# Kernel tuning notes

Hardware: AMD Instinct MI355X
Metric: run time of the kernel (lower is better)

The kernel has to match this reference:

```python
import jax, jax.numpy as jnp
import numpy as np

B, T, W, D = 2, 64, 32, 512
H = 8                      # n_heads
N = 64                     # d_state
EXPAND = 2
DIN = EXPAND * D           # 1024 d_inner
R = -(-D // 16)            # dt_rank = ceil(d_model/16) = 32
K = 4                      # d_conv (mamba default)


def setup_inputs():
    key = jax.random.key(0)
    ks = jax.random.split(key, 20)
    s = 0.02
    inp = {
        'x': jax.random.normal(ks[0], (B, T, W, D), jnp.float32),
        'wq': jax.random.normal(ks[1], (D, D), jnp.float32) * s,
        'bq': jnp.zeros((D,), jnp.float32),
        'wk': jax.random.normal(ks[2], (D, D), jnp.float32) * s,
        'bk': jnp.zeros((D,), jnp.float32),
        'wv': jax.random.normal(ks[3], (D, D), jnp.float32) * s,
        'bv': jnp.zeros((D,), jnp.float32),
        'wo': jax.random.normal(ks[4], (D, D), jnp.float32) * s,
        'bo': jnp.zeros((D,), jnp.float32),
        'in_proj_w': jax.random.normal(ks[5], (2 * DIN, D), jnp.float32) * s,
        'conv_w': jax.random.normal(ks[6], (DIN, 1, K), jnp.float32) * 0.2,
        'conv_b': jnp.zeros((DIN,), jnp.float32),
        'x_proj_w': jax.random.normal(ks[7], (R + 2 * N, DIN), jnp.float32) * s,
        'dt_proj_w': jax.random.normal(ks[8], (DIN, R), jnp.float32) * 0.1,
        'dt_proj_b': jnp.full((DIN,), -4.6, jnp.float32),  # ~softplus^-1(0.01)
        'A_log': jnp.log(jnp.broadcast_to(jnp.arange(1, N + 1, dtype=jnp.float32), (DIN, N))),
        'D_param': jnp.ones((DIN,), jnp.float32),
        'out_proj_w': jax.random.normal(ks[9], (D, DIN), jnp.float32) * s,
        'ln_w': jnp.ones((D,), jnp.float32),
        'ln_b': jnp.zeros((D,), jnp.float32),
    }
    return inp


def _attention(xf, wq, bq, wk, bk, wv, bv, wo, bo):
    b, L, d = xf.shape
    e = d // H
    q = (xf @ wq.T + bq).reshape(b, L, H, e)
    k = (xf @ wk.T + bk).reshape(b, L, H, e)
    v = (xf @ wv.T + bv).reshape(b, L, H, e)
    scale = 1.0 / jnp.sqrt(jnp.float32(e))
    scores = jnp.einsum('blhe,bshe->bhls', q, k) * scale
    causal = jnp.tril(jnp.ones((L, L), bool))
    scores = jnp.where(causal, scores, jnp.finfo(scores.dtype).min)
    attn = jax.nn.softmax(scores, axis=-1)  # dropout off (eval mode)
    out = jnp.einsum('bhls,bshe->blhe', attn, v).reshape(b, L, d)
    return out @ wo.T + bo


def _mamba(xf, in_proj_w, conv_w, conv_b, x_proj_w, dt_proj_w, dt_proj_b,
           A_log, D_param, out_proj_w):
    b, L, d = xf.shape
    xz = xf @ in_proj_w.T                 # (B,L,2*DIN)
    x_in, z = jnp.split(xz, 2, axis=-1)
    # causal depthwise conv1d over L
    xc = jnp.transpose(x_in, (0, 2, 1))   # (B,DIN,L)
    xc = jax.lax.conv_general_dilated(
        xc, conv_w, window_strides=(1,), padding=[(K - 1, 0)],
        feature_group_count=DIN, dimension_numbers=('NCH', 'OIH', 'NCH'))
    xc = xc + conv_b[None, :, None]
    u = jax.nn.silu(jnp.transpose(xc, (0, 2, 1)))   # (B,L,DIN)
    dbc = u @ x_proj_w.T                             # (B,L,R+2N)
    dt, Bm, Cm = dbc[..., :R], dbc[..., R:R + N], dbc[..., R + N:]
    dt = jax.nn.softplus(dt @ dt_proj_w.T + dt_proj_b)  # (B,L,DIN)
    A = -jnp.exp(A_log)                                 # (DIN,N)

    def step(h, t):
        dt_t, B_t, C_t, u_t = t  # (b,DIN),(b,N),(b,N),(b,DIN)
        dA = jnp.exp(dt_t[..., None] * A)                       # (b,DIN,N)
        h = dA * h + (dt_t * u_t)[..., None] * B_t[:, None, :]  # (b,DIN,N)
        y = jnp.einsum('bdn,bn->bd', h, C_t)
        return h, y

    h0 = jnp.zeros((b, DIN, N), xf.dtype)
    xs = (jnp.swapaxes(dt, 0, 1), jnp.swapaxes(Bm, 0, 1),
          jnp.swapaxes(Cm, 0, 1), jnp.swapaxes(u, 0, 1))
    _, ys = jax.lax.scan(step, h0, xs)
    y = jnp.swapaxes(ys, 0, 1) + u * D_param   # (B,L,DIN)
    y = y * jax.nn.silu(z)
    return y @ out_proj_w.T


def reference(x, wq, bq, wk, bk, wv, bv, wo, bo, in_proj_w, conv_w, conv_b,
              x_proj_w, dt_proj_w, dt_proj_b, A_log, D_param, out_proj_w,
              ln_w, ln_b):
    b, t, w, d = x.shape
    L = t * w
    xf = x.reshape(b, L, d)
    x_attn = _attention(xf, wq, bq, wk, bk, wv, bv, wo, bo).reshape(b, t, w, d)
    x_mamba = _mamba(xf, in_proj_w, conv_w, conv_b, x_proj_w, dt_proj_w,
                     dt_proj_b, A_log, D_param, out_proj_w).reshape(b, t, w, d)
    h = x + x_attn + x_mamba
    mu = jnp.mean(h, axis=-1, keepdims=True)
    var = jnp.mean(jnp.square(h - mu), axis=-1, keepdims=True)
    return (h - mu) * jax.lax.rsqrt(var + 1e-5) * ln_w + ln_b
```

## Files before the change

kernel.cpp:

```cpp
#include <hip/hip_runtime.h>

typedef __attribute__((ext_vector_type(4))) float f32x4;
typedef __attribute__((ext_vector_type(8))) short short8;
typedef __attribute__((ext_vector_type(2))) unsigned uint2e;

#define DEV static __device__ __forceinline__

DEV ushort f2b(float f) {
  union { float f; unsigned u; } v; v.f = f;
  unsigned r = v.u + 0x7FFF + ((v.u >> 16) & 1);
  return (ushort)(r >> 16);
}
DEV unsigned pack_bf2(float lo, float hi) {
  return (unsigned)f2b(lo) | ((unsigned)f2b(hi) << 16);
}
DEV float bflo(unsigned p) { return __uint_as_float(p << 16); }
DEV float bfhi(unsigned p) { return __uint_as_float(p & 0xFFFF0000u); }

DEV float fexp2(float x) { float r; asm("v_exp_f32 %0, %1" : "=v"(r) : "v"(x)); return r; }

DEV float xor32_add_lo(float s) {
  uint2e r = __builtin_amdgcn_permlane32_swap(__float_as_uint(s), __float_as_uint(s), false, false);
  return s + __uint_as_float(r.x);
}

#define QP(x, ctrl) __int_as_float(__builtin_amdgcn_update_dpp(0, __float_as_int(x), (ctrl), 0xf, 0xf, false))
#define SWZ(x, off) __int_as_float(__builtin_amdgcn_ds_swizzle(__float_as_int(x), (off)))
#define DPP_ADD(x, ctrl, rmask) \
  ((x) + __int_as_float(__builtin_amdgcn_update_dpp(0, __float_as_int(x), (ctrl), (rmask), 0xf, false)))

#define BB    2
#define LL    2048
#define DD    512
#define HH    8
#define EE    64
#define DIN   1024
#define NS    64
#define RR    32
#define BL    4096
#define NCH   16
#define TC    128
#define NC    1536
#define MFMA(a,b,c) __builtin_amdgcn_mfma_f32_16x16x32_bf16((a),(b),(c),0,0,0)

struct CvtJobs {
  const float* src[7];
  ushort*      dst[7];
  int          n[7];
};

__global__ __launch_bounds__(256) void cvt_multi(CvtJobs j) {
  int job = blockIdx.y;
  const float* s = j.src[job];
  ushort* d = j.dst[job];
  int n = j.n[job];
  for (int i = blockIdx.x * 256 + threadIdx.x; i < n; i += gridDim.x * 256)
    d[i] = f2b(s[i]);
}

__global__ __launch_bounds__(256) void pack_wcomb(
    const float* __restrict__ wo, const float* __restrict__ opw,
    const float* __restrict__ bq, const float* __restrict__ bk,
    const float* __restrict__ bv, ushort* __restrict__ wc,
    float* __restrict__ bqkv)
{
  int i = blockIdx.x * 256 + threadIdx.x;
  if (i < NC) bqkv[i] = (i < DD) ? bq[i] : ((i < 2 * DD) ? bk[i - DD] : bv[i - 2 * DD]);
  if (i >= DD * NC) return;
  int n = i / NC, c = i - n * NC;
  float v = (c < DD) ? wo[n * DD + c] : opw[n * DIN + (c - DD)];
  wc[i] = f2b(v);
}

__global__ __launch_bounds__(256) void gemm_bt(
    const ushort* __restrict__ A, const ushort* __restrict__ W,
    const float* __restrict__ bias, float* __restrict__ outF,
    ushort* __restrict__ outB, int M, int N, int K, int act)
{
  __shared__ ushort As[64][40];
  __shared__ ushort Ws[64][40];
  int m0 = blockIdx.y * 64, n0 = blockIdx.x * 64;
  int tid = threadIdx.x, l = tid & 63, w = tid >> 6;
  int wm = (w >> 1) * 32, wn = (w & 1) * 32;
  int lr = l & 15, kl = (l >> 4) * 8;
  int srow = tid >> 2, sk = (tid & 3) * 8;
  f32x4 acc[2][2] = {};

  for (int k0 = 0; k0 < K; k0 += 32) {
    uint4 av = *(const uint4*)&A[(size_t)(m0 + srow) * K + k0 + sk];
    uint4 wv;
    if (n0 + srow < N) wv = *(const uint4*)&W[(size_t)(n0 + srow) * K + k0 + sk];
    else { wv.x = 0; wv.y = 0; wv.z = 0; wv.w = 0; }
    *(uint4*)&As[srow][sk] = av;
    *(uint4*)&Ws[srow][sk] = wv;
    __syncthreads();
    short8 a0 = *(const short8*)&As[wm + lr][kl];
    short8 a1 = *(const short8*)&As[wm + 16 + lr][kl];
    short8 b0 = *(const short8*)&Ws[wn + lr][kl];
    short8 b1 = *(const short8*)&Ws[wn + 16 + lr][kl];
    acc[0][0] = MFMA(a0, b0, acc[0][0]);
    acc[0][1] = MFMA(a0, b1, acc[0][1]);
    acc[1][0] = MFMA(a1, b0, acc[1][0]);
    acc[1][1] = MFMA(a1, b1, acc[1][1]);
    __syncthreads();
  }

  #pragma unroll
  for (int mi = 0; mi < 2; mi++)
    #pragma unroll
    for (int ni = 0; ni < 2; ni++) {
      int rbase = m0 + wm + mi * 16 + ((l >> 4) << 2);
      int col = n0 + wn + ni * 16 + lr;
      if (col < N) {
        float bval = bias ? bias[col] : 0.f;
        #pragma unroll
        for (int r = 0; r < 4; r++) {
          float v = acc[mi][ni][r] + bval;
          if (act == 1) v = (v > 20.f) ? v : log1pf(__expf(v));
          size_t o = (size_t)(rbase + r) * N + col;
          if (outF) outF[o] = v;
          if (outB) outB[o] = f2b(v);
        }
      }
    }
}

__global__ __launch_bounds__(256) void gemm128(
    const ushort* __restrict__ A, const ushort* __restrict__ W,
    const float* __restrict__ bias, float* __restrict__ outF,
    ushort* __restrict__ outB, int M, int N, int K)
{
  __shared__ ushort As[128][40];
  __shared__ ushort Ws[128][40];
  int tid = threadIdx.x, l = tid & 63, w = tid >> 6;
  int m0 = blockIdx.y * 128, n0 = blockIdx.x * 128;
  int wm = (w >> 1) * 64, wn = (w & 1) * 64;
  int lr = l & 15, kl = (l >> 4) * 8;
  int srow = tid >> 1, sk = (tid & 1) * 16;
  f32x4 acc[4][4] = {};

  const ushort* Ap = A + (size_t)(m0 + srow) * K + sk;
  const ushort* Wp = W + (size_t)(n0 + srow) * K + sk;

  for (int k0 = 0; k0 < K; k0 += 32) {
    uint4 a0 = *(const uint4*)(Ap);
    uint4 a1 = *(const uint4*)(Ap + 8);
    uint4 b0 = *(const uint4*)(Wp);
    uint4 b1 = *(const uint4*)(Wp + 8);
    __syncthreads();
    *(uint4*)&As[srow][sk]     = a0;
    *(uint4*)&As[srow][sk + 8] = a1;
    *(uint4*)&Ws[srow][sk]     = b0;
    *(uint4*)&Ws[srow][sk + 8] = b1;
    __syncthreads();
    short8 af[4], bf[4];
    #pragma unroll
    for (int mi = 0; mi < 4; mi++) af[mi] = *(const short8*)&As[wm + mi * 16 + lr][kl];
    #pragma unroll
    for (int ni = 0; ni < 4; ni++) bf[ni] = *(const short8*)&Ws[wn + ni * 16 + lr][kl];
    #pragma unroll
    for (int mi = 0; mi < 4; mi++)
      #pragma unroll
      for (int ni = 0; ni < 4; ni++)
        acc[mi][ni] = MFMA(af[mi], bf[ni], acc[mi][ni]);
    Ap += 32; Wp += 32;
  }

  #pragma unroll
  for (int mi = 0; mi < 4; mi++)
    #pragma unroll
    for (int ni = 0; ni < 4; ni++) {
      int rbase = m0 + wm + mi * 16 + ((l >> 4) << 2);
      int col = n0 + wn + ni * 16 + lr;
      float bval = bias ? bias[col] : 0.f;
      #pragma unroll
      for (int r = 0; r < 4; r++) {
        float v = acc[mi][ni][r] + bval;
        size_t o = (size_t)(rbase + r) * N + col;
        if (outF) outF[o] = v;
        if (outB) outB[o] = f2b(v);
      }
    }
}

__global__ __launch_bounds__(256) void flash_attn(
    const ushort* __restrict__ qkv, ushort* __restrict__ comb)
{
  __shared__ ushort Qs[64][72];
  __shared__ ushort Ks[64][72];
  __shared__ ushort Vt[64][72];
  __shared__ ushort Ps[64][72];

  int qt = 31 - blockIdx.x;
  int h = blockIdx.y, b = blockIdx.z;
  int tid = threadIdx.x, l = tid & 63, w = tid >> 6;
  int w16 = w * 16, lr = l & 15, kl = (l >> 4) * 8;

  for (int i = tid; i < 512; i += 256) {
    int row = i >> 3, c8 = (i & 7) * 8;
    *(uint4*)&Qs[row][c8] =
        *(const uint4*)&qkv[((size_t)(b * LL + qt * 64 + row)) * NC + h * EE + c8];
  }
  __syncthreads();

  float m_r[4] = {-1e30f, -1e30f, -1e30f, -1e30f};
  float l_r[4] = {0.f, 0.f, 0.f, 0.f};
  f32x4 oacc[4] = {};

  for (int kv = 0; kv <= qt; kv++) {
    for (int i = tid; i < 512; i += 256) {
      int s = i >> 3, c8 = (i & 7) * 8;
      size_t rb = ((size_t)(b * LL + kv * 64 + s)) * NC + h * EE + c8;
      *(uint4*)&Ks[s][c8] = *(const uint4*)&qkv[rb + DD];
      uint4 vv = *(const uint4*)&qkv[rb + 2 * DD];
      const ushort* pv = (const ushort*)&vv;
      #pragma unroll
      for (int jj = 0; jj < 8; jj++) Vt[c8 + jj][s] = pv[jj];
    }
    __syncthreads();

    f32x4 sacc[4] = {};
    #pragma unroll
    for (int kk = 0; kk < 2; kk++) {
      short8 aq = *(const short8*)&Qs[w16 + lr][kk * 32 + kl];
      #pragma unroll
      for (int nt = 0; nt < 4; nt++) {
        short8 bk8 = *(const short8*)&Ks[nt * 16 + lr][kk * 32 + kl];
        sacc[nt] = MFMA(aq, bk8, sacc[nt]);
      }
    }

    bool diag = (kv == qt);
    float scl[4];
    #pragma unroll
    for (int r = 0; r < 4; r++) {
      int rloc = w16 + ((l >> 4) << 2) + r;
      float sv[4];
      #pragma unroll
      for (int nt = 0; nt < 4; nt++) {
        float v = sacc[nt][r] * 0.125f;
        if (diag && (nt * 16 + lr) > rloc) v = -1e30f;
        sv[nt] = v;
      }
      float mx = fmaxf(fmaxf(sv[0], sv[1]), fmaxf(sv[2], sv[3]));
      #pragma unroll
      for (int o = 1; o < 16; o <<= 1) mx = fmaxf(mx, __shfl_xor(mx, o));
      float mnew = fmaxf(m_r[r], mx);
      float sc = __expf(m_r[r] - mnew);
      float rs = 0.f;
      #pragma unroll
      for (int nt = 0; nt < 4; nt++) {
        float p = __expf(sv[nt] - mnew);
        rs += p;
        Ps[rloc][nt * 16 + lr] = f2b(p);
      }
      #pragma unroll
      for (int o = 1; o < 16; o <<= 1) rs += __shfl_xor(rs, o);
      l_r[r] = l_r[r] * sc + rs;
      m_r[r] = mnew;
      scl[r] = sc;
    }
    #pragma unroll
    for (int nt = 0; nt < 4; nt++)
      #pragma unroll
      for (int r = 0; r < 4; r++) oacc[nt][r] *= scl[r];

    #pragma unroll
    for (int kk = 0; kk < 2; kk++) {
      short8 ap = *(const short8*)&Ps[w16 + lr][kk * 32 + kl];
      #pragma unroll
      for (int nt = 0; nt < 4; nt++) {
        short8 bv8 = *(const short8*)&Vt[nt * 16 + lr][kk * 32 + kl];
        oacc[nt] = MFMA(ap, bv8, oacc[nt]);
      }
    }
    __syncthreads();
  }

  #pragma unroll
  for (int nt = 0; nt < 4; nt++)
    #pragma unroll
    for (int r = 0; r < 4; r++) {
      int row = qt * 64 + w16 + ((l >> 4) << 2) + r;
      float v = oacc[nt][r] / l_r[r];
      comb[((size_t)(b * LL + row)) * NC + h * EE + nt * 16 + lr] = f2b(v);
    }
}

__global__ __launch_bounds__(256) void conv_silu(
    const float* __restrict__ xz, const float* __restrict__ cw,
    const float* __restrict__ cb, float* __restrict__ u, ushort* __restrict__ ub)
{
  int i = blockIdx.x * 256 + threadIdx.x;
  if (i >= BL * DIN) return;
  int d = i & (DIN - 1);
  int bl = i >> 10;
  int t = bl & (LL - 1);
  int b = bl >> 11;
  float s = cb[d];
  #pragma unroll
  for (int j = 0; j < 4; j++) {
    int tt = t - 3 + j;
    if (tt >= 0) s += xz[((size_t)(b * LL + tt)) * (2 * DIN) + d] * cw[d * 4 + j];
  }
  float r = s / (1.f + __expf(-s));
  u[i] = r;
  ub[i] = f2b(r);
}

__global__ __launch_bounds__(256) void slice_dt(
    const float* __restrict__ dbc, ushort* __restrict__ dtc)
{
  int i = blockIdx.x * 256 + threadIdx.x;
  if (i >= BL * RR) return;
  int m = i >> 5, r = i & 31;
  dtc[i] = f2b(dbc[m * 160 + r]);
}

__global__ __launch_bounds__(256) void pack_bc(
    const float* __restrict__ dbc, unsigned* __restrict__ bbp,
    float4* __restrict__ bcp4)
{
  int i = blockIdx.x * 256 + threadIdx.x;
  if (i >= BB * (LL / 2) * NS) return;
  int n = i & 63, tp = (i >> 6) & 1023, b = i >> 16;
  size_t r0 = ((size_t)(b * LL + 2 * tp)) * 160;
  float B0 = dbc[r0 + 32 + n],  C0 = dbc[r0 + 96 + n];
  float B1 = dbc[r0 + 192 + n], C1 = dbc[r0 + 256 + n];
  bbp[i] = pack_bf2(B0, B1);
  bcp4[i] = make_float4(B0, C0, B1, C1);
}

__global__ __launch_bounds__(256) void pack_dtu(
    const float* __restrict__ dtf, const float* __restrict__ uf,
    const float* __restrict__ xz, const float* __restrict__ dpar,
    unsigned* __restrict__ dtu_p, unsigned* __restrict__ sg_p)
{
  __shared__ float s_dt[32][65], s_du[32][65], s_gz[32][65], s_ug[32][65];
  int d0 = blockIdx.x * 64, t0 = blockIdx.y * 32;
  int tid = threadIdx.x;
  int c = tid & 63, r4 = tid >> 6;
  float Dv = dpar[d0 + c];
  #pragma unroll
  for (int k = 0; k < 8; k++) {
    int r = k * 4 + r4;
    size_t row = (size_t)(t0 + r);
    float dtv = dtf[row * DIN + d0 + c];
    float uv  = uf [row * DIN + d0 + c];
    float zz  = xz [row * (2 * DIN) + DIN + d0 + c];
    float g = zz / (1.f + __expf(-zz));
    s_dt[r][c] = dtv;
    s_du[r][c] = dtv * uv;
    s_gz[r][c] = g;
    s_ug[r][c] = uv * Dv * g;
  }
  __syncthreads();
  int dl = tid >> 2, q = tid & 3;
  int b = t0 >> 11, tl0 = t0 & (LL - 1);
  size_t obase = ((size_t)(b * DIN + d0 + dl)) * LL + tl0 + q * 8;
  #pragma unroll
  for (int tt = 0; tt < 8; tt++) {
    int t = q * 8 + tt;
    dtu_p[obase + tt] = pack_bf2(s_dt[t][dl], s_du[t][dl]);
    sg_p [obase + tt] = pack_bf2(s_gz[t][dl], s_ug[t][dl]);
  }
}

__global__ __launch_bounds__(256) void scan_phase1(
    const unsigned* __restrict__ dtu_p, const unsigned* __restrict__ bbp,
    const float* __restrict__ alog, float* __restrict__ hf, float* __restrict__ ap)
{
  __shared__ float lds[4][TC][2];
  int tid = threadIdx.x, w = tid >> 6, l = tid & 63;
  int wid = blockIdx.x * 4 + w;
  int d = wid & (DIN - 1);
  int c = (wid >> 10) & (NCH - 1);
  int b = wid >> 14;
  float An2 = -__expf(alog[d * NS + l]) * 1.44269504f;

  size_t pbase = ((size_t)(b * DIN + d)) * LL + c * TC;
  unsigned p0 = dtu_p[pbase + l];
  unsigned p1 = dtu_p[pbase + 64 + l];
  float s0 = bflo(p0), s1 = bflo(p1);
  s0 = DPP_ADD(s0, 0x111, 0xf); s0 = DPP_ADD(s0, 0x112, 0xf);
  s0 = DPP_ADD(s0, 0x114, 0xf); s0 = DPP_ADD(s0, 0x118, 0xf);
  s0 = DPP_ADD(s0, 0x142, 0xa); s0 = DPP_ADD(s0, 0x143, 0xc);
  s1 = DPP_ADD(s1, 0x111, 0xf); s1 = DPP_ADD(s1, 0x112, 0xf);
  s1 = DPP_ADD(s1, 0x114, 0xf); s1 = DPP_ADD(s1, 0x118, 0xf);
  s1 = DPP_ADD(s1, 0x142, 0xa); s1 = DPP_ADD(s1, 0x143, 0xc);
  float T0 = __uint_as_float(__builtin_amdgcn_readlane(__float_as_uint(s0), 63));
  float T  = T0 + __uint_as_float(__builtin_amdgcn_readlane(__float_as_uint(s1), 63));
  lds[w][l][0]      = T - s0;
  lds[w][l][1]      = bfhi(p0);
  lds[w][64 + l][0] = (T - T0) - s1;
  lds[w][64 + l][1] = bfhi(p1);
  __syncthreads();

  const unsigned* bq = bbp + ((size_t)(b * 1024 + c * 64) * 64 + l);
  float h0 = 0.f, h1 = 0.f;
  for (int g = 0; g < 16; g++) {
    unsigned bv[4];
    #pragma unroll
    for (int k = 0; k < 4; k++) bv[k] = bq[k * 64];
    const float* gb = &lds[w][g * 8][0];
    #pragma unroll
    for (int j = 0; j < 8; j++) {
      float2 dd = *(const float2*)(gb + j * 2);
      float Bv = (j & 1) ? bfhi(bv[j >> 1]) : bflo(bv[j >> 1]);
      float a = fexp2(dd.x * An2);
      if (j & 1) h1 += a * (dd.y * Bv);
      else       h0 += a * (dd.y * Bv);
    }
    bq += 256;
  }
  size_t o = (((size_t)((b << 10) + d) * NCH) + c) * 64 + l;
  hf[o] = h0 + h1;
  ap[o] = fexp2(T * An2);
}

__global__ __launch_bounds__(256) void scan_carry(
    const float* __restrict__ hf, const float* __restrict__ ap,
    float* __restrict__ carry)
{
  int i = blockIdx.x * 256 + threadIdx.x;
  int n = i & 63;
  int d = (i >> 6) & (DIN - 1);
  int b = i >> 16;
  size_t base = ((size_t)((b << 10) + d) * NCH) * 64 + n;
  float cur = 0.f;
  #pragma unroll
  for (int c = 0; c < NCH; c++) {
    carry[base + (size_t)c * 64] = cur;
    cur = ap[base + (size_t)c * 64] * cur + hf[base + (size_t)c * 64];
  }
}

__global__ __launch_bounds__(256) void scan_phase3(
    const unsigned* __restrict__ dtu_p, const unsigned* __restrict__ sg_p,
    const float4* __restrict__ bcp4, const float* __restrict__ alog,
    const float* __restrict__ carry, ushort* __restrict__ ymt)
{
  __shared__ float lds[4][TC][4];
  __shared__ ushort yt[4][TC];
  int tid = threadIdx.x, w = tid >> 6, l = tid & 63;
  int wid = blockIdx.x * 4 + w;
  int d = wid & (DIN - 1);
  int c = (wid >> 10) & (NCH - 1);
  int b = wid >> 14;
  float An2 = -__expf(alog[d * NS + l]) * 1.44269504f;

  size_t pbase = ((size_t)(b * DIN + d)) * LL + c * TC;
  #pragma unroll
  for (int q = 0; q < 2; q++) {
    unsigned pd = dtu_p[pbase + q * 64 + l];
    unsigned pg = sg_p [pbase + q * 64 + l];
    lds[w][q * 64 + l][0] = bflo(pd);
    lds[w][q * 64 + l][1] = bfhi(pd);
    lds[w][q * 64 + l][2] = bflo(pg);
    lds[w][q * 64 + l][3] = bfhi(pg);
  }
  __syncthreads();

  float h = carry[(((size_t)((b << 10) + d) * NCH) + c) * 64 + l];
  const float4* bq = bcp4 + ((size_t)(b * 1024 + c * 64) * 64 + l);
  bool s1f = l & 1, s2f = l & 2, s4f = l & 4;
  bool wl = l < 8;

  for (int g = 0; g < 16; g++) {
    float4 bcs[4];
    bcs[0] = bq[0]; bcs[1] = bq[64]; bcs[2] = bq[128]; bcs[3] = bq[192];
    const float* gb = &lds[w][g * 8][0];
    float p[8];
    #pragma unroll
    for (int j = 0; j < 8; j++) {
      float2 dd = *(const float2*)(gb + j * 4);
      float Bv = (j & 1) ? bcs[j >> 1].z : bcs[j >> 1].x;
      float Cv = (j & 1) ? bcs[j >> 1].w : bcs[j >> 1].y;
      float a = fexp2(dd.x * An2);
      h = a * h + dd.y * Bv;
      p[j] = h * Cv;
    }
    #pragma unroll
    for (int j = 0; j < 8; j++) p[j] += QP(p[j], 0xB1);
    float q0 = s1f ? p[1] : p[0];
    float q1 = s1f ? p[3] : p[2];
    float q2 = s1f ? p[5] : p[4];
    float q3 = s1f ? p[7] : p[6];
    q0 += QP(q0, 0x4E); q1 += QP(q1, 0x4E);
    q2 += QP(q2, 0x4E); q3 += QP(q3, 0x4E);
    float r0 = s2f ? q1 : q0;
    float r1 = s2f ? q3 : q2;
    r0 += SWZ(r0, 0x101F); r1 += SWZ(r1, 0x101F);
    float s = s4f ? r1 : r0;
    s += QP(s, 0x128);
    s += SWZ(s, 0x401F);
    s = xor32_add_lo(s);

    float2 sgv = *(const float2*)(&lds[w][g * 8 + (l & 7)][2]);
    if (wl) yt[w][g * 8 + l] = f2b(s * sgv.x + sgv.y);
    bq += 256;
  }
  __syncthreads();
  unsigned vv = *(const unsigned*)&yt[w][2 * l];
  ((unsigned*)(ymt + pbase))[l] = vv;
}

__global__ __launch_bounds__(256) void transpose_ym(
    const ushort* __restrict__ ymt, ushort* __restrict__ comb)
{
  __shared__ ushort tile[64][72];
  int tid = threadIdx.x;
  int bx = blockIdx.x;
  int by = blockIdx.y;
  int b  = blockIdx.z;
  int r = tid >> 2, c16 = (tid & 3) * 16;
  const ushort* src = ymt + ((size_t)(b * DIN + bx * 64 + r)) * LL + by * 64 + c16;
  *(uint4*)&tile[r][c16]     = *(const uint4*)src;
  *(uint4*)&tile[r][c16 + 8] = *(const uint4*)(src + 8);
  __syncthreads();
  ushort tmp[16];
  #pragma unroll
  for (int j = 0; j < 16; j++) tmp[j] = tile[c16 + j][r];
  ushort* dst = comb + ((size_t)(b * LL + by * 64 + r)) * NC + DD + bx * 64 + c16;
  *(uint4*)dst       = *(uint4*)&tmp[0];
  *(uint4*)(dst + 8) = *(uint4*)&tmp[8];
}

__global__ __launch_bounds__(256) void residual_ln(
    const float* __restrict__ x, const float* __restrict__ so,
    const float* __restrict__ lw, const float* __restrict__ lb,
    float* __restrict__ out)
{
  int row = blockIdx.x * 4 + (threadIdx.x >> 6);
  int l = threadIdx.x & 63;
  size_t base = (size_t)row * DD;
  float h[8];
  float s = 0.f, s2 = 0.f;
  #pragma unroll
  for (int half = 0; half < 2; half++) {
    int c = half * 256 + l * 4;
    float4 xv = *(const float4*)(x + base + c);
    float4 sv = *(const float4*)(so + base + c);
    float* hp = h + half * 4;
    hp[0] = xv.x + sv.x;
    hp[1] = xv.y + sv.y;
    hp[2] = xv.z + sv.z;
    hp[3] = xv.w + sv.w;
    #pragma unroll
    for (int j = 0; j < 4; j++) { s += hp[j]; s2 += hp[j] * hp[j]; }
  }
  #pragma unroll
  for (int o = 1; o < 64; o <<= 1) { s += __shfl_xor(s, o); s2 += __shfl_xor(s2, o); }
  float mean = s * (1.f / DD);
  float var = s2 * (1.f / DD) - mean * mean;
  float rs = rsqrtf(var + 1e-5f);
  #pragma unroll
  for (int half = 0; half < 2; half++) {
    int c = half * 256 + l * 4;
    float4 ov;
    ov.x = (h[half*4+0] - mean) * rs * lw[c+0] + lb[c+0];
    ov.y = (h[half*4+1] - mean) * rs * lw[c+1] + lb[c+1];
    ov.z = (h[half*4+2] - mean) * rs * lw[c+2] + lb[c+2];
    ov.w = (h[half*4+3] - mean) * rs * lw[c+3] + lb[c+3];
    *(float4*)(out + base + c) = ov;
  }
}

extern "C" void kernel_launch(void* const* d_in, const int* in_sizes, int n_in,
                              void* d_out, int out_size, void* d_ws, size_t ws_size,
                              hipStream_t stream) {
  const float* x    = (const float*)d_in[0];
  const float* wq   = (const float*)d_in[1];
  const float* bq   = (const float*)d_in[2];
  const float* wk   = (const float*)d_in[3];
  const float* bk   = (const float*)d_in[4];
  const float* wv   = (const float*)d_in[5];
  const float* bv   = (const float*)d_in[6];
  const float* wo   = (const float*)d_in[7];
  const float* bo   = (const float*)d_in[8];
  const float* inw  = (const float*)d_in[9];
  const float* cw   = (const float*)d_in[10];
  const float* cb   = (const float*)d_in[11];
  const float* xpw  = (const float*)d_in[12];
  const float* dtw  = (const float*)d_in[13];
  const float* dtb  = (const float*)d_in[14];
  const float* alog = (const float*)d_in[15];
  const float* dpar = (const float*)d_in[16];
  const float* opw  = (const float*)d_in[17];
  const float* lnw  = (const float*)d_in[18];
  const float* lnb  = (const float*)d_in[19];

  char* ws = (char*)d_ws;
  size_t off = 0;
  auto alloc = [&](size_t bytes) -> void* {
    void* p = ws + off;
    off += (bytes + 255) & ~(size_t)255;
    return p;
  };

  const size_t BLD = (size_t)BL * DD;
  const size_t BLDIN = (size_t)BL * DIN;
  const size_t BLNC = (size_t)BL * NC;

  ushort* xf_b   = (ushort*)alloc(BLD * 2);
  ushort* wqkv_b = (ushort*)alloc((size_t)NC * DD * 2);
  float*  bqkv   = (float*)alloc(NC * 4);
  ushort* inw_b  = (ushort*)alloc(2 * DIN * DD * 2);
  ushort* xpw_b  = (ushort*)alloc(160 * DIN * 2);
  ushort* dtw_b  = (ushort*)alloc(DIN * RR * 2);
  ushort* wcomb_b= (ushort*)alloc((size_t)DD * NC * 2);
  ushort* qkv_b  = (ushort*)alloc(BLNC * 2);
  ushort* comb_a = (ushort*)alloc(BLNC * 2);
  float*  sum_o  = (float*)alloc(BLD * 4);
  float*  xz     = (float*)alloc(BL * (size_t)(2 * DIN) * 4);
  float*  u_f    = (float*)alloc(BLDIN * 4);
  ushort* u_b    = (ushort*)alloc(BLDIN * 2);
  float*  dbc    = (float*)alloc((size_t)BL * 160 * 4);
  ushort* dtc_b  = (ushort*)alloc((size_t)BL * RR * 2);
  float*  dt_f   = (float*)alloc(BLDIN * 4);
  ushort* ymt_b  = (ushort*)alloc(BLDIN * 2);
  unsigned* bbp  = (unsigned*)alloc((size_t)BB * (LL / 2) * NS * 4);
  float4* bcp4   = (float4*)alloc((size_t)BB * (LL / 2) * NS * sizeof(float4));
  unsigned* dtu_p = (unsigned*)alloc(BLDIN * 4);
  unsigned* sg_p  = (unsigned*)alloc(BLDIN * 4);

  const size_t SCN = (size_t)BB * DIN * NCH * 64;
  float* hf_s    = (float*)xz;
  float* ap_s    = hf_s + SCN;
  float* carry_s = ap_s + SCN;

  CvtJobs cj;
  cj.src[0] = x;    cj.dst[0] = xf_b;                 cj.n[0] = (int)BLD;
  cj.src[1] = wq;   cj.dst[1] = wqkv_b;               cj.n[1] = DD * DD;
  cj.src[2] = wk;   cj.dst[2] = wqkv_b + DD * DD;     cj.n[2] = DD * DD;
  cj.src[3] = wv;   cj.dst[3] = wqkv_b + 2 * DD * DD; cj.n[3] = DD * DD;
  cj.src[4] = inw;  cj.dst[4] = inw_b;                cj.n[4] = 2 * DIN * DD;
  cj.src[5] = xpw;  cj.dst[5] = xpw_b;                cj.n[5] = 160 * DIN;
  cj.src[6] = dtw;  cj.dst[6] = dtw_b;                cj.n[6] = DIN * RR;
  cvt_multi<<<dim3(256, 7), 256, 0, stream>>>(cj);
  pack_wcomb<<<dim3((DD * NC + 255) / 256), 256, 0, stream>>>(wo, opw, bq, bk, bv, wcomb_b, bqkv);

  gemm128<<<dim3(12, 32), 256, 0, stream>>>(xf_b, wqkv_b, bqkv, nullptr, qkv_b, BL, NC, DD);

  flash_attn<<<dim3(32, HH, BB), 256, 0, stream>>>(qkv_b, comb_a);

  gemm128<<<dim3(16, 32), 256, 0, stream>>>(xf_b, inw_b, nullptr, xz, nullptr, BL, 2 * DIN, DD);

  conv_silu<<<dim3(32768), 256, 0, stream>>>(xz, cw, cb, u_f, u_b);

  gemm_bt<<<dim3(3, 64), 256, 0, stream>>>(u_b, xpw_b, nullptr, dbc, nullptr, BL, 160, DIN, 0);

  slice_dt<<<dim3(512), 256, 0, stream>>>(dbc, dtc_b);
  gemm_bt<<<dim3(16, 64), 256, 0, stream>>>(dtc_b, dtw_b, dtb, dt_f, nullptr, BL, DIN, RR, 1);

  pack_bc<<<dim3(512), 256, 0, stream>>>(dbc, bbp, bcp4);
  pack_dtu<<<dim3(16, 128), 256, 0, stream>>>(dt_f, u_f, xz, dpar, dtu_p, sg_p);
  scan_phase1<<<dim3(8192), 256, 0, stream>>>(dtu_p, bbp, alog, hf_s, ap_s);
  scan_carry<<<dim3(512), 256, 0, stream>>>(hf_s, ap_s, carry_s);
  scan_phase3<<<dim3(8192), 256, 0, stream>>>(dtu_p, sg_p, bcp4, alog, carry_s, ymt_b);
  transpose_ym<<<dim3(16, 32, BB), 256, 0, stream>>>(ymt_b, comb_a);

  gemm_bt<<<dim3(8, 64), 256, 0, stream>>>(comb_a, wcomb_b, bo, sum_o, nullptr, BL, DD, NC, 0);

  residual_ln<<<dim3(1024), 256, 0, stream>>>(x, sum_o, lnw, lnb, (float*)d_out);
}
```

Baseline: 417.0 us.

## Store mamba intermediates in bf16 and use exp2/DPP reductions in attention softmax

The in_proj GEMM output xz and the dt projection output are now written as bf16 instead of fp32. The fp32 copy of u is dropped, and conv_silu and pack_dtu read the bf16 buffers, which roughly halves memory traffic for these intermediates. Because the smaller xz buffer can no longer hold all the aliased scan scratch, the scan carry buffer gets its own allocation. In flash attention the log2e factor is folded into the score scale so exp2 can be used, and the row max and sum shuffles become DPP/swizzle reductions. The cost is lower precision in the mamba path, since z, u and dt are now rounded to bf16 before the scan.

```diff
diff --git a/kernel.cpp b/kernel.cpp
--- a/kernel.cpp
+++ b/kernel.cpp
@@ -16,6 +16,7 @@
 }
 DEV float bflo(unsigned p) { return __uint_as_float(p << 16); }
 DEV float bfhi(unsigned p) { return __uint_as_float(p & 0xFFFF0000u); }
+DEV float b2f(ushort u) { return __uint_as_float((unsigned)u << 16); }
 
 DEV float fexp2(float x) { float r; asm("v_exp_f32 %0, %1" : "=v"(r) : "v"(x)); return r; }
 
@@ -28,6 +29,8 @@
 #define SWZ(x, off) __int_as_float(__builtin_amdgcn_ds_swizzle(__float_as_int(x), (off)))
 #define DPP_ADD(x, ctrl, rmask) \
   ((x) + __int_as_float(__builtin_amdgcn_update_dpp(0, __float_as_int(x), (ctrl), (rmask), 0xf, false)))
+
+#define LOG2E 1.44269504f
 
 #define BB    2
 #define LL    2048
@@ -206,6 +209,7 @@
   float m_r[4] = {-1e30f, -1e30f, -1e30f, -1e30f};
   float l_r[4] = {0.f, 0.f, 0.f, 0.f};
   f32x4 oacc[4] = {};
+  const float SSC = 0.125f * LOG2E;
 
   for (int kv = 0; kv <= qt; kv++) {
     for (int i = tid; i < 512; i += 256) {
@@ -238,24 +242,28 @@
       float sv[4];
       #pragma unroll
       for (int nt = 0; nt < 4; nt++) {
-        float v = sacc[nt][r] * 0.125f;
+        float v = sacc[nt][r] * SSC;
         if (diag && (nt * 16 + lr) > rloc) v = -1e30f;
         sv[nt] = v;
       }
       float mx = fmaxf(fmaxf(sv[0], sv[1]), fmaxf(sv[2], sv[3]));
-      #pragma unroll
-      for (int o = 1; o < 16; o <<= 1) mx = fmaxf(mx, __shfl_xor(mx, o));
+      mx = fmaxf(mx, QP(mx, 0xB1));
+      mx = fmaxf(mx, QP(mx, 0x4E));
+      mx = fmaxf(mx, SWZ(mx, 0x101F));
+      mx = fmaxf(mx, SWZ(mx, 0x201F));
       float mnew = fmaxf(m_r[r], mx);
-      float sc = __expf(m_r[r] - mnew);
+      float sc = fexp2(m_r[r] - mnew);
       float rs = 0.f;
       #pragma unroll
       for (int nt = 0; nt < 4; nt++) {
-        float p = __expf(sv[nt] - mnew);
+        float p = fexp2(sv[nt] - mnew);
         rs += p;
         Ps[rloc][nt * 16 + lr] = f2b(p);
       }
-      #pragma unroll
-      for (int o = 1; o < 16; o <<= 1) rs += __shfl_xor(rs, o);
+      rs += QP(rs, 0xB1);
+      rs += QP(rs, 0x4E);
+      rs += SWZ(rs, 0x101F);
+      rs += SWZ(rs, 0x201F);
       l_r[r] = l_r[r] * sc + rs;
       m_r[r] = mnew;
       scl[r] = sc;
@@ -288,8 +296,8 @@
 }
 
 __global__ __launch_bounds__(256) void conv_silu(
-    const float* __restrict__ xz, const float* __restrict__ cw,
-    const float* __restrict__ cb, float* __restrict__ u, ushort* __restrict__ ub)
+    const ushort* __restrict__ xz, const float* __restrict__ cw,
+    const float* __restrict__ cb, ushort* __restrict__ ub)
 {
   int i = blockIdx.x * 256 + threadIdx.x;
   if (i >= BL * DIN) return;
@@ -301,10 +309,9 @@
   #pragma unroll
   for (int j = 0; j < 4; j++) {
     int tt = t - 3 + j;
-    if (tt >= 0) s += xz[((size_t)(b * LL + tt)) * (2 * DIN) + d] * cw[d * 4 + j];
+    if (tt >= 0) s += b2f(xz[((size_t)(b * LL + tt)) * (2 * DIN) + d]) * cw[d * 4 + j];
   }
   float r = s / (1.f + __expf(-s));
-  u[i] = r;
   ub[i] = f2b(r);
 }
 
@@ -332,8 +339,8 @@
 }
 
 __global__ __launch_bounds__(256) void pack_dtu(
-    const float* __restrict__ dtf, const float* __restrict__ uf,
-    const float* __restrict__ xz, const float* __restrict__ dpar,
+    const ushort* __restrict__ dtb16, const ushort* __restrict__ ub,
+    const ushort* __restrict__ xz, const float* __restrict__ dpar,
     unsigned* __restrict__ dtu_p, unsigned* __restrict__ sg_p)
 {
   __shared__ float s_dt[32][65], s_du[32][65], s_gz[32][65], s_ug[32][65];
@@ -345,9 +352,9 @@
   for (int k = 0; k < 8; k++) {
     int r = k * 4 + r4;
     size_t row = (size_t)(t0 + r);
-    float dtv = dtf[row * DIN + d0 + c];
-    float uv  = uf [row * DIN + d0 + c];
-    float zz  = xz [row * (2 * DIN) + DIN + d0 + c];
+    float dtv = b2f(dtb16[row * DIN + d0 + c]);
+    float uv  = b2f(ub   [row * DIN + d0 + c]);
+    float zz  = b2f(xz   [row * (2 * DIN) + DIN + d0 + c]);
     float g = zz / (1.f + __expf(-zz));
     s_dt[r][c] = dtv;
     s_du[r][c] = dtv * uv;
@@ -376,7 +383,7 @@
   int d = wid & (DIN - 1);
   int c = (wid >> 10) & (NCH - 1);
   int b = wid >> 14;
-  float An2 = -__expf(alog[d * NS + l]) * 1.44269504f;
+  float An2 = -__expf(alog[d * NS + l]) * LOG2E;
 
   size_t pbase = ((size_t)(b * DIN + d)) * LL + c * TC;
   unsigned p0 = dtu_p[pbase + l];
@@ -447,7 +454,7 @@
   int d = wid & (DIN - 1);
   int c = (wid >> 10) & (NCH - 1);
   int b = wid >> 14;
-  float An2 = -__expf(alog[d * NS + l]) * 1.44269504f;
+  float An2 = -__expf(alog[d * NS + l]) * LOG2E;
 
   size_t pbase = ((size_t)(b * DIN + d)) * LL + c * TC;
   #pragma unroll
@@ -612,12 +619,11 @@
   ushort* qkv_b  = (ushort*)alloc(BLNC * 2);
   ushort* comb_a = (ushort*)alloc(BLNC * 2);
   float*  sum_o  = (float*)alloc(BLD * 4);
-  float*  xz     = (float*)alloc(BL * (size_t)(2 * DIN) * 4);
-  float*  u_f    = (float*)alloc(BLDIN * 4);
+  ushort* xz_b   = (ushort*)alloc(BL * (size_t)(2 * DIN) * 2);
   ushort* u_b    = (ushort*)alloc(BLDIN * 2);
   float*  dbc    = (float*)alloc((size_t)BL * 160 * 4);
   ushort* dtc_b  = (ushort*)alloc((size_t)BL * RR * 2);
-  float*  dt_f   = (float*)alloc(BLDIN * 4);
+  ushort* dt_b   = (ushort*)alloc(BLDIN * 2);
   ushort* ymt_b  = (ushort*)alloc(BLDIN * 2);
   unsigned* bbp  = (unsigned*)alloc((size_t)BB * (LL / 2) * NS * 4);
   float4* bcp4   = (float4*)alloc((size_t)BB * (LL / 2) * NS * sizeof(float4));
@@ -625,9 +631,9 @@
   unsigned* sg_p  = (unsigned*)alloc(BLDIN * 4);
 
   const size_t SCN = (size_t)BB * DIN * NCH * 64;
-  float* hf_s    = (float*)xz;
+  float* hf_s    = (float*)xz_b;
   float* ap_s    = hf_s + SCN;
-  float* carry_s = ap_s + SCN;
+  float* carry_s = (float*)alloc(SCN * 4);
 
   CvtJobs cj;
   cj.src[0] = x;    cj.dst[0] = xf_b;                 cj.n[0] = (int)BLD;
@@ -644,17 +650,17 @@
 
   flash_attn<<<dim3(32, HH, BB), 256, 0, stream>>>(qkv_b, comb_a);
 
-  gemm128<<<dim3(16, 32), 256, 0, stream>>>(xf_b, inw_b, nullptr, xz, nullptr, BL, 2 * DIN, DD);
-
-  conv_silu<<<dim3(32768), 256, 0, stream>>>(xz, cw, cb, u_f, u_b);
+  gemm128<<<dim3(16, 32), 256, 0, stream>>>(xf_b, inw_b, nullptr, nullptr, xz_b, BL, 2 * DIN, DD);
+
+  conv_silu<<<dim3(32768), 256, 0, stream>>>(xz_b, cw, cb, u_b);
 
   gemm_bt<<<dim3(3, 64), 256, 0, stream>>>(u_b, xpw_b, nullptr, dbc, nullptr, BL, 160, DIN, 0);
 
   slice_dt<<<dim3(512), 256, 0, stream>>>(dbc, dtc_b);
-  gemm_bt<<<dim3(16, 64), 256, 0, stream>>>(dtc_b, dtw_b, dtb, dt_f, nullptr, BL, DIN, RR, 1);
+  gemm_bt<<<dim3(16, 64), 256, 0, stream>>>(dtc_b, dtw_b, dtb, nullptr, dt_b, BL, DIN, RR, 1);
 
   pack_bc<<<dim3(512), 256, 0, stream>>>(dbc, bbp, bcp4);
-  pack_dtu<<<dim3(16, 128), 256, 0, stream>>>(dt_f, u_f, xz, dpar, dtu_p, sg_p);
+  pack_dtu<<<dim3(16, 128), 256, 0, stream>>>(dt_b, u_b, xz_b, dpar, dtu_p, sg_p);
   scan_phase1<<<dim3(8192), 256, 0, stream>>>(dtu_p, bbp, alog, hf_s, ap_s);
   scan_carry<<<dim3(512), 256, 0, stream>>>(hf_s, ap_s, carry_s);
   scan_phase3<<<dim3(8192), 256, 0, stream>>>(dtu_p, sg_p, bcp4, alog, carry_s, ymt_b);
```

Result: faster. 398.5 us (-4.4%).
